# Performance work log

Hardware: AMD Instinct MI355X
Metric: run time of the kernel (lower is better)

Reference implementation:

```python
import jax, jax.numpy as jnp
import numpy as np

N = 50000      # nodes
E = 1000000    # edges
R = 16         # relations
NB = 16        # bases = min(30, R)
D = 128        # entity/hidden/output dim
V = 500000     # entities
L = 3          # layers
G = 64         # graphs in batch
EPS = 1e-5


def setup_inputs() -> dict:
    key = jax.random.key(0)
    ks = jax.random.split(key, 11)
    node_ids = jax.random.randint(ks[0], (N,), 0, V)
    edge_index = jax.random.randint(ks[1], (2, E), 0, N)
    edge_type = jax.random.randint(ks[2], (E,), 0, R)
    batch = jnp.sort(jax.random.randint(ks[3], (N,), 0, G))
    emb = (jax.random.normal(ks[4], (V, D), jnp.float32) * 0.02).at[0].set(0.0)  # padding_idx=0
    comp = jax.random.normal(ks[5], (L, R, NB), jnp.float32) / np.sqrt(NB).astype(np.float32)
    basis = jax.random.normal(ks[6], (L, NB, D, D), jnp.float32) / np.sqrt(D).astype(np.float32)
    root = jax.random.normal(ks[7], (L, D, D), jnp.float32) / np.sqrt(D).astype(np.float32)
    bias = jnp.zeros((L, D), jnp.float32)
    gamma = jnp.ones((L, D), jnp.float32)
    beta = jnp.zeros((L, D), jnp.float32)
    return {"node_ids": node_ids, "edge_index": edge_index, "edge_type": edge_type,
            "batch": batch, "emb": emb, "comp": comp, "basis": basis, "root": root,
            "bias": bias, "gamma": gamma, "beta": beta}


def _rgcn_layer(x, src, dst, seg, comp_l, basis_l, root_l, bias_l, inv_cnt):
    # Per-relation mean aggregation: mean-then-transform == transform-then-mean (linear).
    msum = jax.ops.segment_sum(x[src], seg, num_segments=N * R)       # [N*R, D]
    mean = (msum * inv_cnt).reshape(N, R, -1)                          # [N, R, D]
    W = jnp.einsum('rb,bio->rio', comp_l, basis_l)                     # [R, D, D]
    return jnp.einsum('nri,rio->no', mean, W) + x @ root_l + bias_l


def _layernorm(x, g, b):
    mu = jnp.mean(x, axis=-1, keepdims=True)
    var = jnp.mean(jnp.square(x - mu), axis=-1, keepdims=True)
    return (x - mu) * jax.lax.rsqrt(var + EPS) * g + b


def reference(node_ids, edge_index, edge_type, batch, emb, comp, basis, root, bias, gamma, beta):
    src, dst = edge_index[0], edge_index[1]
    seg = dst * R + edge_type                                          # [(node, relation)] segment id
    cnt = jax.ops.segment_sum(jnp.ones((E,), jnp.float32), seg, num_segments=N * R)
    inv_cnt = (1.0 / jnp.maximum(cnt, 1.0))[:, None]                   # [N*R, 1]
    x = emb[node_ids]                                                  # [N, D]
    for l in range(L):
        x_new = _rgcn_layer(x, src, dst, seg, comp[l], basis[l], root[l], bias[l], inv_cnt)
        x_new = jax.nn.relu(_layernorm(x_new, gamma[l], beta[l]))      # dropout = identity (eval)
        x = x + x_new                                                  # dims match every layer
    gsum = jax.ops.segment_sum(x, batch, num_segments=G)               # global_mean_pool
    gcnt = jax.ops.segment_sum(jnp.ones((N,), jnp.float32), batch, num_segments=G)
    graph_embedding = gsum / jnp.maximum(gcnt, 1.0)[:, None]
    return x, graph_embedding
```

## Files before the change

kernel.cpp:

```cpp
#include <hip/hip_runtime.h>
#include <hip/hip_bf16.h>

#define N_ 50000
#define E_ 1000000
#define R_ 16
#define NB_ 16
#define D_ 128
#define L_ 3
#define G_ 64
#define M_SEG (N_*R_)
#define KTOT ((R_+1)*D_)
#define SCAN_BLOCKS ((M_SEG + 1023)/1024)
#define MAXM 450000
#define GM 128

typedef _Float16 f16;
typedef _Float16 f16x8 __attribute__((ext_vector_type(8)));
typedef _Float16 f16x4 __attribute__((ext_vector_type(4)));
typedef float f32x4 __attribute__((ext_vector_type(4)));


__global__ __launch_bounds__(256) void k_hist(const int* __restrict__ ei, const int* __restrict__ et,
                                              int* __restrict__ cnt){
  int e = blockIdx.x*256 + threadIdx.x;
  if (e < E_){
    int seg = ei[E_ + e]*R_ + et[e];
    atomicAdd(&cnt[seg], 1);
  }
}

__global__ __launch_bounds__(256) void k_scan_sum(const int* __restrict__ cnt, int* __restrict__ bsum){
  __shared__ int sh[256];
  int base = blockIdx.x*1024 + threadIdx.x*4;
  int s = 0;
  #pragma unroll
  for (int j=0;j<4;++j){ int i = base + j; if (i < M_SEG) s += cnt[i]; }
  sh[threadIdx.x] = s; __syncthreads();
  for (int off=128; off>0; off>>=1){
    if (threadIdx.x < off) sh[threadIdx.x] += sh[threadIdx.x+off];
    __syncthreads();
  }
  if (threadIdx.x==0) bsum[blockIdx.x] = sh[0];
}

__global__ __launch_bounds__(256) void k_scan_off(const int* __restrict__ bsum, int* __restrict__ boff){
  __shared__ int sh[256];
  int tid = threadIdx.x;
  int v[4]; int ts = 0;
  #pragma unroll
  for (int j=0;j<4;++j){ int i = tid*4+j; v[j] = (i<SCAN_BLOCKS)? bsum[i] : 0; ts += v[j]; }
  sh[tid] = ts; __syncthreads();
  for (int off=1; off<256; off<<=1){
    int a = sh[tid];
    int b = (tid>=off)? sh[tid-off] : 0;
    __syncthreads(); sh[tid] = a + b; __syncthreads();
  }
  int excl = sh[tid] - ts;
  #pragma unroll
  for (int j=0;j<4;++j){ int i = tid*4+j; if (i<SCAN_BLOCKS) boff[i] = excl; excl += v[j]; }
}

__global__ __launch_bounds__(256) void k_scan_write(const int* __restrict__ cnt, const int* __restrict__ boff,
                                                    int* __restrict__ row_ptr, int* __restrict__ cursor,
                                                    float* __restrict__ inv){
  __shared__ int sh[256];
  int tid = threadIdx.x;
  int base = blockIdx.x*1024 + tid*4;
  int v[4]; int ts = 0;
  #pragma unroll
  for (int j=0;j<4;++j){ int i = base+j; v[j] = (i<M_SEG)? cnt[i] : 0; ts += v[j]; }
  sh[tid] = ts; __syncthreads();
  for (int off=1; off<256; off<<=1){
    int a = sh[tid];
    int b = (tid>=off)? sh[tid-off] : 0;
    __syncthreads(); sh[tid] = a + b; __syncthreads();
  }
  int excl = boff[blockIdx.x] + sh[tid] - ts;
  #pragma unroll
  for (int j=0;j<4;++j){
    int i = base+j;
    if (i < M_SEG){
      row_ptr[i] = excl; cursor[i] = excl;
      int c = v[j];
      inv[i] = 1.0f / (float)(c > 1 ? c : 1);
      if (i == M_SEG-1) row_ptr[M_SEG] = excl + c;
    }
    excl += v[j];
  }
}

__global__ __launch_bounds__(256) void k_place(const int* __restrict__ ei, const int* __restrict__ et,
                                               int* __restrict__ cursor, int* __restrict__ csr_src){
  int e = blockIdx.x*256 + threadIdx.x;
  if (e < E_){
    int seg = ei[E_+e]*R_ + et[e];
    int pos = atomicAdd(&cursor[seg], 1);
    csr_src[pos] = ei[e];
  }
}

__global__ __launch_bounds__(256) void k_idx(const int* __restrict__ cnt, const int* __restrict__ row_ptr,
                                             const int* __restrict__ csr_src,
                                             int* __restrict__ idxT, int* __restrict__ mlist,
                                             int* __restrict__ mcount){
  int i = blockIdx.x*256 + threadIdx.x;
  if (i < M_SEG){
    int n = i >> 4, r = i & 15;
    int c = cnt[i];
    int v;
    if (c == 0) v = 1;
    else if (c == 1) v = csr_src[row_ptr[i]] << 1;
    else {
      int slot = atomicAdd(mcount, 1);
      if (slot < MAXM){ mlist[slot] = i; v = ((1 + slot) << 1) | 1; }
      else v = 1;
    }
    idxT[r*N_ + n] = v;
  } else if (i < M_SEG + N_){
    int n = i - M_SEG;
    idxT[16*N_ + n] = n << 1;
  }
}


__global__ __launch_bounds__(128) void k_gather(const int* __restrict__ ids, const float* __restrict__ emb,
                                                float* __restrict__ x, f16* __restrict__ x16){
  int t = threadIdx.x;
  int n = blockIdx.x*4 + (t >> 5);
  int c = (t & 31) * 4;
  if (n < N_){
    int id = ids[n];
    float4 v = *(const float4*)(emb + (size_t)id*D_ + c);
    *(float4*)(x + (size_t)n*D_ + c) = v;
    f16x4 h = {(f16)v.x, (f16)v.y, (f16)v.z, (f16)v.w};
    *(f16x4*)(x16 + (size_t)n*D_ + c) = h;
  }
}

__global__ __launch_bounds__(128) void k_wprep(const float* __restrict__ comp, const float* __restrict__ basis,
                                               const float* __restrict__ root, f16* __restrict__ Wt){
  int b = blockIdx.x;
  int o = threadIdx.x;
  int l = b / ((R_+1)*D_);
  int rem = b % ((R_+1)*D_);
  int r = rem / D_;
  int i = rem % D_;
  float acc = 0.f;
  if (r < R_){
    #pragma unroll
    for (int bb=0; bb<NB_; ++bb)
      acc += comp[(l*R_+r)*NB_+bb] * basis[((l*NB_+bb)*D_+i)*D_+o];
  } else {
    acc = root[(l*D_+i)*D_+o];
  }
  Wt[(size_t)l*D_*KTOT + (size_t)o*KTOT + r*D_ + i] = (f16)acc;
}

__global__ __launch_bounds__(256) void k_means(const f16* __restrict__ x16,
                                               const int* __restrict__ row_ptr, const int* __restrict__ csr_src,
                                               const float* __restrict__ inv,
                                               const int* __restrict__ mlist, const int* __restrict__ mcount,
                                               f16* __restrict__ abuf){
  int grp = (blockIdx.x*256 + threadIdx.x) >> 5;
  int l32 = threadIdx.x & 31;
  int mc = *mcount; if (mc > MAXM) mc = MAXM;
  int ngrp = gridDim.x * 8;
  for (int slot = grp; slot < mc; slot += ngrp){
    int seg = mlist[slot];
    int p0 = row_ptr[seg], p1 = row_ptr[seg+1];
    float a0=0.f,a1=0.f,a2=0.f,a3=0.f;
    float b0=0.f,b1=0.f,b2=0.f,b3=0.f;
    int p = p0;
    for (; p + 1 < p1; p += 2){
      int s0 = csr_src[p], s1 = csr_src[p+1];
      f16x4 v0 = *(const f16x4*)(x16 + (size_t)s0*D_ + l32*4);
      f16x4 v1 = *(const f16x4*)(x16 + (size_t)s1*D_ + l32*4);
      a0 += (float)v0[0]; a1 += (float)v0[1]; a2 += (float)v0[2]; a3 += (float)v0[3];
      b0 += (float)v1[0]; b1 += (float)v1[1]; b2 += (float)v1[2]; b3 += (float)v1[3];
    }
    if (p < p1){
      int s0 = csr_src[p];
      f16x4 v0 = *(const f16x4*)(x16 + (size_t)s0*D_ + l32*4);
      a0 += (float)v0[0]; a1 += (float)v0[1]; a2 += (float)v0[2]; a3 += (float)v0[3];
    }
    float ic = inv[seg];
    f16x4 o = {(f16)((a0+b0)*ic), (f16)((a1+b1)*ic), (f16)((a2+b2)*ic), (f16)((a3+b3)*ic)};
    *(f16x4*)(abuf + (size_t)(1+slot)*D_ + l32*4) = o;
  }
}

__global__ __launch_bounds__(256) void k_gemm(
    const int* __restrict__ idxT, const f16* __restrict__ x16, const f16* __restrict__ abuf,
    const f16* __restrict__ Wt, const float* __restrict__ xin,
    const float* __restrict__ bias, const float* __restrict__ gamma, const float* __restrict__ beta,
    float* __restrict__ xout, f16* __restrict__ xout16)
{
  const int tid  = threadIdx.x;
  const int lane = tid & 63;
  const int wave = tid >> 6;
  const int l15  = lane & 15;
  const int quad = lane >> 4;
  const int nbase = blockIdx.x * GM;

  f32x4 acc[2][8];
  f32x4 z = {0.f,0.f,0.f,0.f};
  #pragma unroll
  for (int h=0;h<2;++h)
    #pragma unroll
    for (int nt=0;nt<8;++nt) acc[h][nt] = z;

  int nodeh[2];
  #pragma unroll
  for (int h=0;h<2;++h) nodeh[h] = nbase + (wave*2 + h)*16 + l15;

  const f16* wp[8];
  #pragma unroll
  for (int nt=0;nt<8;++nt)
    wp[nt] = Wt + (size_t)(nt*16 + l15)*KTOT + quad*8;

  int aidx[2];
  #pragma unroll
  for (int h=0;h<2;++h) aidx[h] = (nodeh[h] < N_) ? idxT[nodeh[h]] : 1;

  for (int r = 0; r < R_+1; ++r){
    const f16* ab[2];
    #pragma unroll
    for (int h=0;h<2;++h)
      ab[h] = ((aidx[h] & 1) ? abuf : x16) + (size_t)(aidx[h] >> 1) * D_ + quad*8;

    if (r < R_){
      #pragma unroll
      for (int h=0;h<2;++h) aidx[h] = (nodeh[h] < N_) ? idxT[(r+1)*N_ + nodeh[h]] : 1;
    }

    #pragma unroll
    for (int ks = 0; ks < 4; ++ks){
      f16x8 af0 = *(const f16x8*)(ab[0] + ks*32);
      f16x8 af1 = *(const f16x8*)(ab[1] + ks*32);
      #pragma unroll
      for (int nt = 0; nt < 8; ++nt){
        f16x8 bf = *(const f16x8*)(wp[nt] + ks*32);
        acc[0][nt] = __builtin_amdgcn_mfma_f32_16x16x32_f16(af0, bf, acc[0][nt], 0, 0, 0);
        acc[1][nt] = __builtin_amdgcn_mfma_f32_16x16x32_f16(af1, bf, acc[1][nt], 0, 0, 0);
      }
    }
    #pragma unroll
    for (int nt=0;nt<8;++nt) wp[nt] += D_;
  }

  float bv[8], gv[8], btv[8];
  #pragma unroll
  for (int nt=0;nt<8;++nt){
    int col = nt*16 + l15;
    bv[nt] = bias[col]; gv[nt] = gamma[col]; btv[nt] = beta[col];
  }
  #pragma unroll
  for (int h=0;h<2;++h){
    #pragma unroll
    for (int j=0;j<4;++j){
      int rowl = (wave*2 + h)*16 + quad*4 + j;
      int node = nbase + rowl;
      float t[8]; float s=0.f, s2=0.f;
      #pragma unroll
      for (int nt=0;nt<8;++nt){
        float v = acc[h][nt][j] + bv[nt];
        t[nt] = v; s += v; s2 += v*v;
      }
      #pragma unroll
      for (int m=1;m<16;m<<=1){ s += __shfl_xor(s,m,64); s2 += __shfl_xor(s2,m,64); }
      float mu  = s * (1.f/128.f);
      float var = s2 * (1.f/128.f) - mu*mu;
      float rs  = rsqrtf(var + 1e-5f);
      if (node < N_){
        #pragma unroll
        for (int nt=0;nt<8;++nt){
          int col = nt*16 + l15;
          float o = (t[nt]-mu)*rs*gv[nt] + btv[nt];
          o = fmaxf(o, 0.f);
          float res = xin[(size_t)node*D_ + col] + o;
          xout[(size_t)node*D_ + col] = res;
          xout16[(size_t)node*D_ + col] = (f16)res;
        }
      }
    }
  }
}


__device__ __forceinline__ int lbound_batch(const int* __restrict__ b, int key){
  int lo=0, hi=N_;
  while (lo<hi){ int mid=(lo+hi)>>1; if (b[mid]<key) lo=mid+1; else hi=mid; }
  return lo;
}

__global__ __launch_bounds__(256) void k_pool(const float* __restrict__ x, const int* __restrict__ batch,
                                              float* __restrict__ gout){
  __shared__ float sh[256];
  int g = blockIdx.x;
  int a = lbound_batch(batch, g);
  int b = lbound_batch(batch, g+1);
  int t = threadIdx.x;
  int d = t & 127, half = t >> 7;
  float s = 0.f;
  for (int n = a + half; n < b; n += 2) s += x[(size_t)n*D_ + d];
  sh[t] = s; __syncthreads();
  if (half == 0){
    float tot = sh[t] + sh[t+128];
    int c = b - a;
    gout[g*D_ + d] = tot / (float)(c > 1 ? c : 1);
  }
}


extern "C" void kernel_launch(void* const* d_in, const int* in_sizes, int n_in,
                              void* d_out, int out_size, void* d_ws, size_t ws_size,
                              hipStream_t stream){
  const int*   node_ids = (const int*)d_in[0];
  const int*   ei       = (const int*)d_in[1];
  const int*   et       = (const int*)d_in[2];
  const int*   batch    = (const int*)d_in[3];
  const float* emb      = (const float*)d_in[4];
  const float* comp     = (const float*)d_in[5];
  const float* basis    = (const float*)d_in[6];
  const float* root     = (const float*)d_in[7];
  const float* bias     = (const float*)d_in[8];
  const float* gamma    = (const float*)d_in[9];
  const float* beta     = (const float*)d_in[10];
  float* out = (float*)d_out;

  char* ws = (char*)d_ws;
  size_t off = 0;
  auto alloc = [&](size_t bytes) -> void* {
    void* p = ws + off;
    off = (off + bytes + 255) & ~(size_t)255;
    return p;
  };
  int*   cnt     = (int*)  alloc((size_t)M_SEG*4);
  int*   row_ptr = (int*)  alloc(((size_t)M_SEG+1)*4);
  int*   cursor  = (int*)  alloc((size_t)M_SEG*4);
  float* invc    = (float*)alloc((size_t)M_SEG*4);
  int*   csr_src = (int*)  alloc((size_t)E_*4);
  int*   bsum    = (int*)  alloc((size_t)SCAN_BLOCKS*4);
  int*   boff    = (int*)  alloc((size_t)SCAN_BLOCKS*4);
  int*   idxT    = (int*)  alloc((size_t)(R_+1)*N_*4);
  int*   mlist   = (int*)  alloc((size_t)MAXM*4);
  int*   mcount  = (int*)  alloc(256);
  float* xA      = (float*)alloc((size_t)N_*D_*4);
  float* xB      = (float*)alloc((size_t)N_*D_*4);
  f16*   xA16    = (f16*)  alloc((size_t)N_*D_*2);
  f16*   xB16    = (f16*)  alloc((size_t)N_*D_*2);
  f16*   Wt      = (f16*)  alloc((size_t)L_*D_*KTOT*2);
  f16*   abuf    = (f16*)  alloc((size_t)(MAXM+1)*D_*2);

  hipMemsetAsync(cnt, 0, (size_t)M_SEG*4, stream);
  hipMemsetAsync(mcount, 0, 256, stream);
  hipMemsetAsync(abuf, 0, (size_t)D_*2, stream);

  k_hist      <<<(E_+255)/256, 256, 0, stream>>>(ei, et, cnt);
  k_scan_sum  <<<SCAN_BLOCKS, 256, 0, stream>>>(cnt, bsum);
  k_scan_off  <<<1, 256, 0, stream>>>(bsum, boff);
  k_scan_write<<<SCAN_BLOCKS, 256, 0, stream>>>(cnt, boff, row_ptr, cursor, invc);
  k_place     <<<(E_+255)/256, 256, 0, stream>>>(ei, et, cursor, csr_src);
  k_idx       <<<(M_SEG+N_+255)/256, 256, 0, stream>>>(cnt, row_ptr, csr_src, idxT, mlist, mcount);
  k_gather    <<<(N_+3)/4, 128, 0, stream>>>(node_ids, emb, xA, xA16);
  k_wprep     <<<L_*(R_+1)*D_, 128, 0, stream>>>(comp, basis, root, Wt);

  const int GB = (N_ + GM - 1)/GM;
  k_means<<<4096, 256, 0, stream>>>(xA16, row_ptr, csr_src, invc, mlist, mcount, abuf);
  k_gemm <<<GB, 256, 0, stream>>>(idxT, xA16, abuf, Wt + (size_t)0*D_*KTOT, xA,
                                  bias+0*D_, gamma+0*D_, beta+0*D_, xB, xB16);
  k_means<<<4096, 256, 0, stream>>>(xB16, row_ptr, csr_src, invc, mlist, mcount, abuf);
  k_gemm <<<GB, 256, 0, stream>>>(idxT, xB16, abuf, Wt + (size_t)1*D_*KTOT, xB,
                                  bias+1*D_, gamma+1*D_, beta+1*D_, xA, xA16);
  k_means<<<4096, 256, 0, stream>>>(xA16, row_ptr, csr_src, invc, mlist, mcount, abuf);
  k_gemm <<<GB, 256, 0, stream>>>(idxT, xA16, abuf, Wt + (size_t)2*D_*KTOT, xA,
                                  bias+2*D_, gamma+2*D_, beta+2*D_, out, xB16);

  k_pool <<<G_, 256, 0, stream>>>(out, batch, out + (size_t)N_*D_);
}
```

Baseline: 1.315 ms.

## Split GEMM output columns across waves, widen mean gathers, precompute multi-edge segment info

```diff
diff --git a/kernel.cpp b/kernel.cpp
--- a/kernel.cpp
+++ b/kernel.cpp
@@ -12,7 +12,7 @@
 #define KTOT ((R_+1)*D_)
 #define SCAN_BLOCKS ((M_SEG + 1023)/1024)
 #define MAXM 450000
-#define GM 128
+#define GM 64
 
 typedef _Float16 f16;
 typedef _Float16 f16x8 __attribute__((ext_vector_type(8)));
@@ -61,8 +61,7 @@
 }
 
 __global__ __launch_bounds__(256) void k_scan_write(const int* __restrict__ cnt, const int* __restrict__ boff,
-                                                    int* __restrict__ row_ptr, int* __restrict__ cursor,
-                                                    float* __restrict__ inv){
+                                                    int* __restrict__ row_ptr, int* __restrict__ cursor){
   __shared__ int sh[256];
   int tid = threadIdx.x;
   int base = blockIdx.x*1024 + tid*4;
@@ -81,9 +80,7 @@
     int i = base+j;
     if (i < M_SEG){
       row_ptr[i] = excl; cursor[i] = excl;
-      int c = v[j];
-      inv[i] = 1.0f / (float)(c > 1 ? c : 1);
-      if (i == M_SEG-1) row_ptr[M_SEG] = excl + c;
+      if (i == M_SEG-1) row_ptr[M_SEG] = excl + v[j];
     }
     excl += v[j];
   }
@@ -101,7 +98,8 @@
 
 __global__ __launch_bounds__(256) void k_idx(const int* __restrict__ cnt, const int* __restrict__ row_ptr,
                                              const int* __restrict__ csr_src,
-                                             int* __restrict__ idxT, int* __restrict__ mlist,
+                                             int* __restrict__ idxT, int* __restrict__ mp0,
+                                             int* __restrict__ mpc, float* __restrict__ minv,
                                              int* __restrict__ mcount){
   int i = blockIdx.x*256 + threadIdx.x;
   if (i < M_SEG){
@@ -112,7 +110,10 @@
     else if (c == 1) v = csr_src[row_ptr[i]] << 1;
     else {
       int slot = atomicAdd(mcount, 1);
-      if (slot < MAXM){ mlist[slot] = i; v = ((1 + slot) << 1) | 1; }
+      if (slot < MAXM){
+        mp0[slot] = row_ptr[i]; mpc[slot] = c; minv[slot] = 1.0f/(float)c;
+        v = ((1 + slot) << 1) | 1;
+      }
       else v = 1;
     }
     idxT[r*N_ + n] = v;
@@ -157,35 +158,40 @@
 }
 
 __global__ __launch_bounds__(256) void k_means(const f16* __restrict__ x16,
-                                               const int* __restrict__ row_ptr, const int* __restrict__ csr_src,
-                                               const float* __restrict__ inv,
-                                               const int* __restrict__ mlist, const int* __restrict__ mcount,
+                                               const int* __restrict__ csr_src,
+                                               const int* __restrict__ mp0, const int* __restrict__ mpc,
+                                               const float* __restrict__ minv, const int* __restrict__ mcount,
                                                f16* __restrict__ abuf){
-  int grp = (blockIdx.x*256 + threadIdx.x) >> 5;
-  int l32 = threadIdx.x & 31;
+  int grp = (blockIdx.x*256 + threadIdx.x) >> 4;
+  int l16 = threadIdx.x & 15;
   int mc = *mcount; if (mc > MAXM) mc = MAXM;
-  int ngrp = gridDim.x * 8;
+  int ngrp = gridDim.x * 16;
   for (int slot = grp; slot < mc; slot += ngrp){
-    int seg = mlist[slot];
-    int p0 = row_ptr[seg], p1 = row_ptr[seg+1];
-    float a0=0.f,a1=0.f,a2=0.f,a3=0.f;
-    float b0=0.f,b1=0.f,b2=0.f,b3=0.f;
+    int p0 = mp0[slot];
+    int c  = mpc[slot];
+    float ic = minv[slot];
+    int p1 = p0 + c;
+    float a0=0.f,a1=0.f,a2=0.f,a3=0.f,a4=0.f,a5=0.f,a6=0.f,a7=0.f;
+    float b0=0.f,b1=0.f,b2=0.f,b3=0.f,b4=0.f,b5=0.f,b6=0.f,b7=0.f;
     int p = p0;
     for (; p + 1 < p1; p += 2){
       int s0 = csr_src[p], s1 = csr_src[p+1];
-      f16x4 v0 = *(const f16x4*)(x16 + (size_t)s0*D_ + l32*4);
-      f16x4 v1 = *(const f16x4*)(x16 + (size_t)s1*D_ + l32*4);
-      a0 += (float)v0[0]; a1 += (float)v0[1]; a2 += (float)v0[2]; a3 += (float)v0[3];
-      b0 += (float)v1[0]; b1 += (float)v1[1]; b2 += (float)v1[2]; b3 += (float)v1[3];
+      f16x8 v0 = *(const f16x8*)(x16 + (size_t)s0*D_ + l16*8);
+      f16x8 v1 = *(const f16x8*)(x16 + (size_t)s1*D_ + l16*8);
+      a0+=(float)v0[0]; a1+=(float)v0[1]; a2+=(float)v0[2]; a3+=(float)v0[3];
+      a4+=(float)v0[4]; a5+=(float)v0[5]; a6+=(float)v0[6]; a7+=(float)v0[7];
+      b0+=(float)v1[0]; b1+=(float)v1[1]; b2+=(float)v1[2]; b3+=(float)v1[3];
+      b4+=(float)v1[4]; b5+=(float)v1[5]; b6+=(float)v1[6]; b7+=(float)v1[7];
     }
     if (p < p1){
       int s0 = csr_src[p];
-      f16x4 v0 = *(const f16x4*)(x16 + (size_t)s0*D_ + l32*4);
-      a0 += (float)v0[0]; a1 += (float)v0[1]; a2 += (float)v0[2]; a3 += (float)v0[3];
-    }
-    float ic = inv[seg];
-    f16x4 o = {(f16)((a0+b0)*ic), (f16)((a1+b1)*ic), (f16)((a2+b2)*ic), (f16)((a3+b3)*ic)};
-    *(f16x4*)(abuf + (size_t)(1+slot)*D_ + l32*4) = o;
+      f16x8 v0 = *(const f16x8*)(x16 + (size_t)s0*D_ + l16*8);
+      a0+=(float)v0[0]; a1+=(float)v0[1]; a2+=(float)v0[2]; a3+=(float)v0[3];
+      a4+=(float)v0[4]; a5+=(float)v0[5]; a6+=(float)v0[6]; a7+=(float)v0[7];
+    }
+    f16x8 o = {(f16)((a0+b0)*ic),(f16)((a1+b1)*ic),(f16)((a2+b2)*ic),(f16)((a3+b3)*ic),
+               (f16)((a4+b4)*ic),(f16)((a5+b5)*ic),(f16)((a6+b6)*ic),(f16)((a7+b7)*ic)};
+    *(f16x8*)(abuf + (size_t)(1+slot)*D_ + l16*8) = o;
   }
 }
 
@@ -195,87 +201,98 @@
     const float* __restrict__ bias, const float* __restrict__ gamma, const float* __restrict__ beta,
     float* __restrict__ xout, f16* __restrict__ xout16)
 {
+  __shared__ float2 part[GM][4];
+
   const int tid  = threadIdx.x;
   const int lane = tid & 63;
   const int wave = tid >> 6;
   const int l15  = lane & 15;
   const int quad = lane >> 4;
   const int nbase = blockIdx.x * GM;
-
-  f32x4 acc[2][8];
+  const int colb = wave * 32;
+
+  f32x4 acc[4][2];
   f32x4 z = {0.f,0.f,0.f,0.f};
   #pragma unroll
-  for (int h=0;h<2;++h)
-    #pragma unroll
-    for (int nt=0;nt<8;++nt) acc[h][nt] = z;
-
-  int nodeh[2];
-  #pragma unroll
-  for (int h=0;h<2;++h) nodeh[h] = nbase + (wave*2 + h)*16 + l15;
-
-  const f16* wp[8];
-  #pragma unroll
-  for (int nt=0;nt<8;++nt)
-    wp[nt] = Wt + (size_t)(nt*16 + l15)*KTOT + quad*8;
-
-  int aidx[2];
-  #pragma unroll
-  for (int h=0;h<2;++h) aidx[h] = (nodeh[h] < N_) ? idxT[nodeh[h]] : 1;
+  for (int h=0;h<4;++h){ acc[h][0] = z; acc[h][1] = z; }
+
+  int nodeh[4];
+  #pragma unroll
+  for (int h=0;h<4;++h) nodeh[h] = nbase + h*16 + l15;
+
+  const f16* wp0 = Wt + (size_t)(colb + l15)*KTOT + quad*8;
+  const f16* wp1 = Wt + (size_t)(colb + 16 + l15)*KTOT + quad*8;
+
+  int aidx[4];
+  #pragma unroll
+  for (int h=0;h<4;++h) aidx[h] = (nodeh[h] < N_) ? idxT[nodeh[h]] : 1;
 
   for (int r = 0; r < R_+1; ++r){
-    const f16* ab[2];
-    #pragma unroll
-    for (int h=0;h<2;++h)
+    const f16* ab[4];
+    #pragma unroll
+    for (int h=0;h<4;++h)
       ab[h] = ((aidx[h] & 1) ? abuf : x16) + (size_t)(aidx[h] >> 1) * D_ + quad*8;
 
     if (r < R_){
       #pragma unroll
-      for (int h=0;h<2;++h) aidx[h] = (nodeh[h] < N_) ? idxT[(r+1)*N_ + nodeh[h]] : 1;
+      for (int h=0;h<4;++h) aidx[h] = (nodeh[h] < N_) ? idxT[(r+1)*N_ + nodeh[h]] : 1;
     }
 
     #pragma unroll
     for (int ks = 0; ks < 4; ++ks){
-      f16x8 af0 = *(const f16x8*)(ab[0] + ks*32);
-      f16x8 af1 = *(const f16x8*)(ab[1] + ks*32);
+      f16x8 bf0 = *(const f16x8*)(wp0 + ks*32);
+      f16x8 bf1 = *(const f16x8*)(wp1 + ks*32);
       #pragma unroll
-      for (int nt = 0; nt < 8; ++nt){
-        f16x8 bf = *(const f16x8*)(wp[nt] + ks*32);
-        acc[0][nt] = __builtin_amdgcn_mfma_f32_16x16x32_f16(af0, bf, acc[0][nt], 0, 0, 0);
-        acc[1][nt] = __builtin_amdgcn_mfma_f32_16x16x32_f16(af1, bf, acc[1][nt], 0, 0, 0);
+      for (int h = 0; h < 4; ++h){
+        f16x8 af = *(const f16x8*)(ab[h] + ks*32);
+        acc[h][0] = __builtin_amdgcn_mfma_f32_16x16x32_f16(af, bf0, acc[h][0], 0, 0, 0);
+        acc[h][1] = __builtin_amdgcn_mfma_f32_16x16x32_f16(af, bf1, acc[h][1], 0, 0, 0);
       }
     }
-    #pragma unroll
-    for (int nt=0;nt<8;++nt) wp[nt] += D_;
-  }
-
-  float bv[8], gv[8], btv[8];
-  #pragma unroll
-  for (int nt=0;nt<8;++nt){
-    int col = nt*16 + l15;
+    wp0 += D_; wp1 += D_;
+  }
+
+  float bv[2], gv[2], btv[2];
+  #pragma unroll
+  for (int nt=0;nt<2;++nt){
+    int col = colb + nt*16 + l15;
     bv[nt] = bias[col]; gv[nt] = gamma[col]; btv[nt] = beta[col];
   }
   #pragma unroll
-  for (int h=0;h<2;++h){
+  for (int h=0;h<4;++h){
     #pragma unroll
     for (int j=0;j<4;++j){
-      int rowl = (wave*2 + h)*16 + quad*4 + j;
-      int node = nbase + rowl;
-      float t[8]; float s=0.f, s2=0.f;
-      #pragma unroll
-      for (int nt=0;nt<8;++nt){
-        float v = acc[h][nt][j] + bv[nt];
-        t[nt] = v; s += v; s2 += v*v;
-      }
+      float t0 = acc[h][0][j] + bv[0];
+      float t1 = acc[h][1][j] + bv[1];
+      float s  = t0 + t1;
+      float s2 = t0*t0 + t1*t1;
       #pragma unroll
       for (int m=1;m<16;m<<=1){ s += __shfl_xor(s,m,64); s2 += __shfl_xor(s2,m,64); }
+      if (l15 == 0){
+        int row = h*16 + quad*4 + j;
+        part[row][wave] = make_float2(s, s2);
+      }
+    }
+  }
+  __syncthreads();
+  #pragma unroll
+  for (int h=0;h<4;++h){
+    #pragma unroll
+    for (int j=0;j<4;++j){
+      int row = h*16 + quad*4 + j;
+      int node = nbase + row;
+      float2 p0 = part[row][0], p1 = part[row][1], p2 = part[row][2], p3 = part[row][3];
+      float s  = p0.x + p1.x + p2.x + p3.x;
+      float s2 = p0.y + p1.y + p2.y + p3.y;
       float mu  = s * (1.f/128.f);
       float var = s2 * (1.f/128.f) - mu*mu;
       float rs  = rsqrtf(var + 1e-5f);
       if (node < N_){
         #pragma unroll
-        for (int nt=0;nt<8;++nt){
-          int col = nt*16 + l15;
-          float o = (t[nt]-mu)*rs*gv[nt] + btv[nt];
+        for (int nt=0;nt<2;++nt){
+          int col = colb + nt*16 + l15;
+          float v = acc[h][nt][j] + bv[nt];
+          float o = (v-mu)*rs*gv[nt] + btv[nt];
           o = fmaxf(o, 0.f);
           float res = xin[(size_t)node*D_ + col] + o;
           xout[(size_t)node*D_ + col] = res;
@@ -338,12 +355,13 @@
   int*   cnt     = (int*)  alloc((size_t)M_SEG*4);
   int*   row_ptr = (int*)  alloc(((size_t)M_SEG+1)*4);
   int*   cursor  = (int*)  alloc((size_t)M_SEG*4);
-  float* invc    = (float*)alloc((size_t)M_SEG*4);
   int*   csr_src = (int*)  alloc((size_t)E_*4);
   int*   bsum    = (int*)  alloc((size_t)SCAN_BLOCKS*4);
   int*   boff    = (int*)  alloc((size_t)SCAN_BLOCKS*4);
   int*   idxT    = (int*)  alloc((size_t)(R_+1)*N_*4);
-  int*   mlist   = (int*)  alloc((size_t)MAXM*4);
+  int*   mp0     = (int*)  alloc((size_t)MAXM*4);
+  int*   mpc     = (int*)  alloc((size_t)MAXM*4);
+  float* minv    = (float*)alloc((size_t)MAXM*4);
   int*   mcount  = (int*)  alloc(256);
   float* xA      = (float*)alloc((size_t)N_*D_*4);
   float* xB      = (float*)alloc((size_t)N_*D_*4);
@@ -359,20 +377,20 @@
   k_hist      <<<(E_+255)/256, 256, 0, stream>>>(ei, et, cnt);
   k_scan_sum  <<<SCAN_BLOCKS, 256, 0, stream>>>(cnt, bsum);
   k_scan_off  <<<1, 256, 0, stream>>>(bsum, boff);
-  k_scan_write<<<SCAN_BLOCKS, 256, 0, stream>>>(cnt, boff, row_ptr, cursor, invc);
+  k_scan_write<<<SCAN_BLOCKS, 256, 0, stream>>>(cnt, boff, row_ptr, cursor);
   k_place     <<<(E_+255)/256, 256, 0, stream>>>(ei, et, cursor, csr_src);
-  k_idx       <<<(M_SEG+N_+255)/256, 256, 0, stream>>>(cnt, row_ptr, csr_src, idxT, mlist, mcount);
+  k_idx       <<<(M_SEG+N_+255)/256, 256, 0, stream>>>(cnt, row_ptr, csr_src, idxT, mp0, mpc, minv, mcount);
   k_gather    <<<(N_+3)/4, 128, 0, stream>>>(node_ids, emb, xA, xA16);
   k_wprep     <<<L_*(R_+1)*D_, 128, 0, stream>>>(comp, basis, root, Wt);
 
   const int GB = (N_ + GM - 1)/GM;
-  k_means<<<4096, 256, 0, stream>>>(xA16, row_ptr, csr_src, invc, mlist, mcount, abuf);
+  k_means<<<4096, 256, 0, stream>>>(xA16, csr_src, mp0, mpc, minv, mcount, abuf);
   k_gemm <<<GB, 256, 0, stream>>>(idxT, xA16, abuf, Wt + (size_t)0*D_*KTOT, xA,
                                   bias+0*D_, gamma+0*D_, beta+0*D_, xB, xB16);
-  k_means<<<4096, 256, 0, stream>>>(xB16, row_ptr, csr_src, invc, mlist, mcount, abuf);
+  k_means<<<4096, 256, 0, stream>>>(xB16, csr_src, mp0, mpc, minv, mcount, abuf);
   k_gemm <<<GB, 256, 0, stream>>>(idxT, xB16, abuf, Wt + (size_t)1*D_*KTOT, xB,
                                   bias+1*D_, gamma+1*D_, beta+1*D_, xA, xA16);
-  k_means<<<4096, 256, 0, stream>>>(xA16, row_ptr, csr_src, invc, mlist, mcount, abuf);
+  k_means<<<4096, 256, 0, stream>>>(xA16, csr_src, mp0, mpc, minv, mcount, abuf);
   k_gemm <<<GB, 256, 0, stream>>>(idxT, xA16, abuf, Wt + (size_t)2*D_*KTOT, xA,
                                   bias+2*D_, gamma+2*D_, beta+2*D_, out, xB16);
 
```

Result: slower. 1.347 ms (+2.4%).
